# Kernel tuning notes

Measured on AMD Instinct MI355X. Metric: run time of the kernel, lower is better.

## Reference

```python
import jax, jax.numpy as jnp
import numpy as np

N_HEAD = 16

def apply_rope(t, cos, sin):
    # t: [B, H, T, hd]; cos/sin: [T, hd//2] -> broadcast [1,1,T,hd//2]
    hd = t.shape[-1]
    t1, t2 = t[..., : hd // 2], t[..., hd // 2 :]
    c = cos[None, None, :, :]
    s = sin[None, None, :, :]
    return jnp.concatenate([t1 * c - t2 * s, t1 * s + t2 * c], axis=-1)

def setup_inputs() -> dict:
    key = jax.random.key(0)
    k1, k2, k3, k4, k5 = jax.random.split(key, 5)
    B, T, C = 2, 2048, 2048
    hd = C // N_HEAD
    x = jax.random.normal(k1, (B, T, C), dtype=jnp.float32)
    cos = jax.random.uniform(k2, (T, hd // 2), dtype=jnp.float32)
    sin = jax.random.uniform(k3, (T, hd // 2), dtype=jnp.float32)
    W_attn = jax.random.normal(k4, (C, 3 * C), dtype=jnp.float32) * (1.0 / np.sqrt(C))
    W_proj = jax.random.normal(k5, (C, C), dtype=jnp.float32) * (1.0 / np.sqrt(C))
    return {"x": x, "cos": cos, "sin": sin, "W_attn": W_attn, "W_proj": W_proj}

def reference(x, cos, sin, W_attn, W_proj):
    B, T, C = x.shape
    hd = C // N_HEAD
    qkv = jnp.einsum("btc,cd->btd", x, W_attn)  # [B,T,3C]
    q, k, v = jnp.split(qkv, 3, axis=-1)
    # [B,T,C] -> [B,H,T,hd]
    def to_heads(t):
        return t.reshape(B, T, N_HEAD, hd).transpose(0, 2, 1, 3)
    q, k, v = to_heads(q), to_heads(k), to_heads(v)
    q = apply_rope(q, cos[:T], sin[:T])
    k = apply_rope(k, cos[:T], sin[:T])
    scale = 1.0 / np.sqrt(hd).astype(np.float32)
    scores = jnp.einsum("bhqd,bhkd->bhqk", q, k) * scale
    causal = jnp.tril(jnp.ones((T, T), dtype=bool))
    scores = jnp.where(causal[None, None], scores, jnp.finfo(scores.dtype).min)
    attn = jax.nn.softmax(scores, axis=-1)
    y = jnp.einsum("bhqk,bhkd->bhqd", attn, v)  # [B,H,T,hd]
    y = y.transpose(0, 2, 1, 3).reshape(B, T, C)
    return jnp.einsum("btc,cd->btd", y, W_proj)
```

## Files before the change

kernel.cpp:

```cpp
#include <hip/hip_runtime.h>
#include <stdint.h>

typedef unsigned short u16;
typedef __bf16 v8bf __attribute__((ext_vector_type(8)));
typedef float f32x4 __attribute__((ext_vector_type(4)));

#define MFMA16(a, b, c) __builtin_amdgcn_mfma_f32_16x16x32_bf16((a), (b), (c), 0, 0, 0)

typedef const __attribute__((address_space(1))) uint32_t* gp32;
typedef __attribute__((address_space(3))) uint32_t* lp32;
#define ASYNC16(g, l) __builtin_amdgcn_global_load_lds((gp32)(const void*)(g), (lp32)(void*)(l), 16, 0, 0)

__device__ __forceinline__ u16 f2bf(float f) {
  union { float f; uint32_t u; } v; v.f = f;
  uint32_t r = v.u + 0x7fffu + ((v.u >> 16) & 1u);
  return (u16)(r >> 16);
}
__device__ __forceinline__ float bf2f(u16 h) {
  union { uint32_t u; float f; } v; v.u = ((uint32_t)h) << 16;
  return v.f;
}

__device__ __forceinline__ int swK(int r, int lc) {
  return r * 128 + (((lc ^ (r & 7)) & 15) << 3);
}
__device__ __forceinline__ int swV(int r, int lc) {
  return r * 64 + (((lc ^ (r & 7)) & 7) << 3);
}

__global__ __launch_bounds__(256) void cast_x_kernel(const float* __restrict__ in,
                                                     u16* __restrict__ out) {
  int i = (blockIdx.x * 256 + threadIdx.x) * 8;
  float4 a = *(const float4*)(in + i);
  float4 b = *(const float4*)(in + i + 4);
  uint4 o;
  o.x = (uint32_t)f2bf(a.x) | ((uint32_t)f2bf(a.y) << 16);
  o.y = (uint32_t)f2bf(a.z) | ((uint32_t)f2bf(a.w) << 16);
  o.z = (uint32_t)f2bf(b.x) | ((uint32_t)f2bf(b.y) << 16);
  o.w = (uint32_t)f2bf(b.z) | ((uint32_t)f2bf(b.w) << 16);
  *(uint4*)(out + i) = o;
}

__global__ __launch_bounds__(256) void transpose_cast_kernel(const float* __restrict__ in,
                                                             u16* __restrict__ out,
                                                             int R, int Cc) {
  __shared__ u16 tile[32][34];
  int c0 = blockIdx.x * 32, r0 = blockIdx.y * 32;
  int tx = threadIdx.x, ty = threadIdx.y;
#pragma unroll
  for (int i = 0; i < 32; i += 8)
    tile[ty + i][tx] = f2bf(in[(size_t)(r0 + ty + i) * Cc + c0 + tx]);
  __syncthreads();
#pragma unroll
  for (int i = 0; i < 32; i += 8)
    out[(size_t)(c0 + ty + i) * R + r0 + tx] = tile[tx][ty + i];
}

template <typename OutT>
__global__ __launch_bounds__(256) void gemm_bt(const u16* __restrict__ A,
                                               const u16* __restrict__ Bt,
                                               OutT* __restrict__ C, int M, int N, int K) {
  __shared__ u16 As[128 * 64];
  __shared__ u16 Bs[128 * 64];
  int tid = threadIdx.x;
  int wave = tid >> 6, lane = tid & 63, quad = lane >> 4, l16 = lane & 15;
  int wr = wave >> 1, wc = wave & 1;
  int m0 = blockIdx.y * 128, n0 = blockIdx.x * 128;
  f32x4 acc[4][4] = {};
  int lrow = lane >> 3, lk = lane & 7;
  int lc = lk ^ lrow;
  const u16* Ab = A + (size_t)m0 * K;
  const u16* Bb = Bt + (size_t)n0 * K;

  for (int k0 = 0; k0 < K; k0 += 64) {
#pragma unroll
    for (int j = 0; j < 4; ++j) {
      int rbase = wave * 32 + j * 8;
      int row = rbase + lrow;
      ASYNC16(Ab + (size_t)row * K + k0 + lc * 8, &As[rbase * 64]);
      ASYNC16(Bb + (size_t)row * K + k0 + lc * 8, &Bs[rbase * 64]);
    }
    __syncthreads();
#pragma unroll
    for (int ks = 0; ks < 2; ++ks) {
      v8bf af[4], bfr[4];
#pragma unroll
      for (int t = 0; t < 4; ++t) {
        af[t]  = *(const v8bf*)&As[swV(wr * 64 + t * 16 + l16, ks * 4 + quad)];
        bfr[t] = *(const v8bf*)&Bs[swV(wc * 64 + t * 16 + l16, ks * 4 + quad)];
      }
#pragma unroll
      for (int mt = 0; mt < 4; ++mt)
#pragma unroll
        for (int nt = 0; nt < 4; ++nt)
          acc[mt][nt] = MFMA16(af[mt], bfr[nt], acc[mt][nt]);
    }
    __syncthreads();
  }
#pragma unroll
  for (int mt = 0; mt < 4; ++mt)
#pragma unroll
    for (int nt = 0; nt < 4; ++nt) {
      int row = m0 + wr * 64 + mt * 16 + quad * 4;
      int col = n0 + wc * 64 + nt * 16 + l16;
#pragma unroll
      for (int r = 0; r < 4; ++r) {
        float v = acc[mt][nt][r];
        if constexpr (sizeof(OutT) == 2)
          C[(size_t)(row + r) * N + col] = (OutT)f2bf(v);
        else
          C[(size_t)(row + r) * N + col] = v;
      }
    }
}

__global__ __launch_bounds__(256) void rope_repack(const u16* __restrict__ qkv,
                                                   const float* __restrict__ cosp,
                                                   const float* __restrict__ sinp,
                                                   u16* __restrict__ qh, u16* __restrict__ kh,
                                                   u16* __restrict__ vt) {
  __shared__ u16 tile[128 * 130];
  const int T = 2048, C3 = 6144;
  const float QSCL = 0.08838834764831845f * 1.4426950408889634f;
  int t0 = blockIdx.x * 128;
  int bh = blockIdx.y, b = bh >> 4, h = bh & 15;
  int tid = threadIdx.x;
#pragma unroll 2
  for (int i = 0; i < 32; ++i) {
    int e = i * 256 + tid;
    int tl = e >> 6, j = e & 63;
    int t = t0 + tl;
    size_t base = (size_t)(b * T + t) * C3 + h * 128;
    float c = cosp[t * 64 + j], s = sinp[t * 64 + j];
    float q1 = bf2f(qkv[base + j]),        q2 = bf2f(qkv[base + 64 + j]);
    float k1 = bf2f(qkv[base + 2048 + j]), k2 = bf2f(qkv[base + 2048 + 64 + j]);
    size_t o = ((size_t)bh * T + t) * 128;
    qh[o + j]      = f2bf((q1 * c - q2 * s) * QSCL);
    qh[o + 64 + j] = f2bf((q1 * s + q2 * c) * QSCL);
    kh[o + j]      = f2bf(k1 * c - k2 * s);
    kh[o + 64 + j] = f2bf(k1 * s + k2 * c);
  }
#pragma unroll 2
  for (int i = 0; i < 32; ++i) {
    int e = i * 256 + tid;
    int tl = e >> 6, dc = (e & 63) * 2;
    size_t base = (size_t)(b * T + t0 + tl) * C3 + 4096 + h * 128;
    *(uint32_t*)&tile[tl * 130 + dc] = *(const uint32_t*)&qkv[base + dc];
  }
  __syncthreads();
#pragma unroll 2
  for (int i = 0; i < 32; ++i) {
    int e = i * 256 + tid;
    int d = e >> 6, tp = (e & 63) * 2;
    uint32_t v = (uint32_t)tile[tp * 130 + d] | ((uint32_t)tile[(tp + 1) * 130 + d] << 16);
    *(uint32_t*)&vt[((size_t)bh * 128 + d) * T + t0 + tp] = v;
  }
}

__global__ __launch_bounds__(256) void flash_attn(const u16* __restrict__ qh,
                                                  const u16* __restrict__ kh,
                                                  const u16* __restrict__ vt,
                                                  u16* __restrict__ yh) {
  __shared__ u16 Ks[2][64 * 128];
  __shared__ u16 Vs[128 * 64];
  __shared__ u16 Pb[128 * 64];
  const int T = 2048, HD = 128;
  int tid = threadIdx.x;
  int wave = tid >> 6, lane = tid & 63, quad = lane >> 4, l16 = lane & 15;
  int bh = blockIdx.y, b = bh >> 4, h = bh & 15;
  const u16* qb = qh + (size_t)bh * T * HD;
  const u16* kb = kh + (size_t)bh * T * HD;
  const u16* vb = vt + (size_t)bh * HD * T;
  int krow_off = lane >> 4, kchunk = lane & 15;
  int vrow_off = lane >> 3, vchunk = lane & 7;

  for (int tp = 0; tp < 2; ++tp) {
    int qt = tp ? 15 - (int)blockIdx.x : (int)blockIdx.x;
    int q0 = qt * 128;
    int n_it = 2 * qt + 2;

    v8bf qf[2][4];
#pragma unroll
    for (int mt = 0; mt < 2; ++mt)
#pragma unroll
      for (int ks = 0; ks < 4; ++ks)
        qf[mt][ks] = *(const v8bf*)&qb[(size_t)(q0 + wave * 32 + mt * 16 + l16) * HD + ks * 32 + quad * 8];

    f32x4 acc[2][8] = {};
    float rs_p[2][4] = {};
    uint4 vreg[4];

#pragma unroll
    for (int j = 0; j < 4; ++j) {
      int rbase = wave * 16 + j * 4;
      int r = rbase + krow_off;
      int lc = kchunk ^ (r & 7);
      ASYNC16(kb + (size_t)r * HD + lc * 8, &Ks[0][rbase * 128]);
    }
#pragma unroll
    for (int j = 0; j < 4; ++j) {
      int row = wave * 32 + j * 8 + vrow_off;
      int lc = vchunk ^ (row & 7);
      vreg[j] = *(const uint4*)&vb[(size_t)row * T + lc * 8];
    }
    __syncthreads();
#pragma unroll
    for (int j = 0; j < 4; ++j) {
      int row = wave * 32 + j * 8 + vrow_off;
      *(uint4*)&Vs[row * 64 + vchunk * 8] = vreg[j];
    }

    for (int it = 0; it < n_it; ++it) {
      int c = it & 1;
      __syncthreads();

      if (it + 1 < n_it) {
        int kv0n = (it + 1) * 64;
#pragma unroll
        for (int j = 0; j < 4; ++j) {
          int rbase = wave * 16 + j * 4;
          int r = rbase + krow_off;
          int lc = kchunk ^ (r & 7);
          ASYNC16(kb + (size_t)(kv0n + r) * HD + lc * 8, &Ks[1 - c][rbase * 128]);
        }
#pragma unroll
        for (int j = 0; j < 4; ++j) {
          int row = wave * 32 + j * 8 + vrow_off;
          int lc = vchunk ^ (row & 7);
          vreg[j] = *(const uint4*)&vb[(size_t)row * T + kv0n + lc * 8];
        }
      }

      f32x4 s[2][4] = {};
#pragma unroll
      for (int ks = 0; ks < 4; ++ks)
#pragma unroll
        for (int nt = 0; nt < 4; ++nt) {
          v8bf kf = *(const v8bf*)&Ks[c][swK(nt * 16 + l16, ks * 4 + quad)];
          s[0][nt] = MFMA16(qf[0][ks], kf, s[0][nt]);
          s[1][nt] = MFMA16(qf[1][ks], kf, s[1][nt]);
        }

      if (it >= 2 * qt) {
        int kv0 = it * 64;
#pragma unroll
        for (int mt = 0; mt < 2; ++mt)
#pragma unroll
          for (int r = 0; r < 4; ++r) {
            int row = q0 + wave * 32 + mt * 16 + quad * 4 + r;
#pragma unroll
            for (int nt = 0; nt < 4; ++nt)
              if (kv0 + nt * 16 + l16 > row) s[mt][nt][r] = -1e30f;
          }
      }

#pragma unroll
      for (int mt = 0; mt < 2; ++mt)
#pragma unroll
        for (int nt = 0; nt < 4; ++nt)
#pragma unroll
          for (int r = 0; r < 4; ++r) {
            float p = __builtin_exp2f(s[mt][nt][r]);
            rs_p[mt][r] += p;
            int row = wave * 32 + mt * 16 + quad * 4 + r;
            int col = nt * 16 + l16;
            Pb[row * 64 + ((((col >> 3) ^ (row & 7)) & 7) << 3) + (col & 7)] = f2bf(p);
          }

#pragma unroll
      for (int ks = 0; ks < 2; ++ks) {
        v8bf pa0 = *(const v8bf*)&Pb[swV(wave * 32 + l16, ks * 4 + quad)];
        v8bf pa1 = *(const v8bf*)&Pb[swV(wave * 32 + 16 + l16, ks * 4 + quad)];
#pragma unroll
        for (int dt = 0; dt < 8; ++dt) {
          v8bf vf = *(const v8bf*)&Vs[swV(dt * 16 + l16, ks * 4 + quad)];
          acc[0][dt] = MFMA16(pa0, vf, acc[0][dt]);
          acc[1][dt] = MFMA16(pa1, vf, acc[1][dt]);
        }
      }

      __syncthreads();

      if (it + 1 < n_it) {
#pragma unroll
        for (int j = 0; j < 4; ++j) {
          int row = wave * 32 + j * 8 + vrow_off;
          *(uint4*)&Vs[row * 64 + vchunk * 8] = vreg[j];
        }
      }
    }

#pragma unroll
    for (int mt = 0; mt < 2; ++mt)
#pragma unroll
      for (int r = 0; r < 4; ++r) {
        float rsv = rs_p[mt][r];
        rsv += __shfl_xor(rsv, 1);
        rsv += __shfl_xor(rsv, 2);
        rsv += __shfl_xor(rsv, 4);
        rsv += __shfl_xor(rsv, 8);
        float inv = 1.f / rsv;
        int t = q0 + wave * 32 + mt * 16 + quad * 4 + r;
#pragma unroll
        for (int dt = 0; dt < 8; ++dt)
          yh[(size_t)(b * T + t) * 2048 + h * 128 + dt * 16 + l16] = f2bf(acc[mt][dt][r] * inv);
      }
  }
}

extern "C" void kernel_launch(void* const* d_in, const int* in_sizes, int n_in,
                              void* d_out, int out_size, void* d_ws, size_t ws_size,
                              hipStream_t stream) {
  const float* x    = (const float*)d_in[0];
  const float* cosp = (const float*)d_in[1];
  const float* sinp = (const float*)d_in[2];
  const float* Wa   = (const float*)d_in[3];
  const float* Wp   = (const float*)d_in[4];
  float* out = (float*)d_out;

  char* ws = (char*)d_ws;
  u16* xb  = (u16*)(ws);
  u16* WaT = (u16*)(ws + (size_t)(16 << 20));
  u16* WpT = (u16*)(ws + (size_t)(40 << 20));
  u16* qkv = (u16*)(ws + (size_t)(48 << 20));
  u16* qh  = (u16*)(ws + (size_t)(96 << 20));
  u16* kh  = (u16*)(ws + (size_t)(112 << 20));
  u16* vt  = (u16*)(ws + (size_t)(128 << 20));
  u16* yh  = (u16*)(ws + (size_t)(144 << 20));

  cast_x_kernel<<<4096, 256, 0, stream>>>(x, xb);
  transpose_cast_kernel<<<dim3(192, 64), dim3(32, 8), 0, stream>>>(Wa, WaT, 2048, 6144);
  transpose_cast_kernel<<<dim3(64, 64), dim3(32, 8), 0, stream>>>(Wp, WpT, 2048, 2048);
  gemm_bt<u16><<<dim3(48, 32), 256, 0, stream>>>(xb, WaT, qkv, 4096, 6144, 2048);
  rope_repack<<<dim3(16, 32), 256, 0, stream>>>(qkv, cosp, sinp, qh, kh, vt);
  flash_attn<<<dim3(8, 32), 256, 0, stream>>>(qh, kh, vt, yh);
  gemm_bt<float><<<dim3(16, 32), 256, 0, stream>>>(yh, WpT, out, 4096, 2048, 2048);
}
```

Baseline: 427.5 us.

## Split flash attention KV range across two wave groups per block

```diff
diff --git a/kernel.cpp b/kernel.cpp
--- a/kernel.cpp
+++ b/kernel.cpp
@@ -157,77 +157,83 @@
   }
 }
 
-__global__ __launch_bounds__(256) void flash_attn(const u16* __restrict__ qh,
+__global__ __launch_bounds__(512) void flash_attn(const u16* __restrict__ qh,
                                                   const u16* __restrict__ kh,
                                                   const u16* __restrict__ vt,
                                                   u16* __restrict__ yh) {
-  __shared__ u16 Ks[2][64 * 128];
-  __shared__ u16 Vs[128 * 64];
-  __shared__ u16 Pb[128 * 64];
+  __shared__ u16 L[2][32768];
   const int T = 2048, HD = 128;
   int tid = threadIdx.x;
-  int wave = tid >> 6, lane = tid & 63, quad = lane >> 4, l16 = lane & 15;
+  int g = tid >> 8;
+  int gwave = (tid >> 6) & 3;
+  int lane = tid & 63, quad = lane >> 4, l16 = lane & 15;
   int bh = blockIdx.y, b = bh >> 4, h = bh & 15;
   const u16* qb = qh + (size_t)bh * T * HD;
   const u16* kb = kh + (size_t)bh * T * HD;
   const u16* vb = vt + (size_t)bh * HD * T;
+  u16* Ks0 = &L[g][0];
+  u16* Ks1 = &L[g][8192];
+  u16* Vs  = &L[g][16384];
+  u16* Pb  = &L[g][24576];
   int krow_off = lane >> 4, kchunk = lane & 15;
   int vrow_off = lane >> 3, vchunk = lane & 7;
 
   for (int tp = 0; tp < 2; ++tp) {
     int qt = tp ? 15 - (int)blockIdx.x : (int)blockIdx.x;
     int q0 = qt * 128;
-    int n_it = 2 * qt + 2;
+    int n_it = qt + 1;
 
     v8bf qf[2][4];
 #pragma unroll
     for (int mt = 0; mt < 2; ++mt)
 #pragma unroll
       for (int ks = 0; ks < 4; ++ks)
-        qf[mt][ks] = *(const v8bf*)&qb[(size_t)(q0 + wave * 32 + mt * 16 + l16) * HD + ks * 32 + quad * 8];
+        qf[mt][ks] = *(const v8bf*)&qb[(size_t)(q0 + gwave * 32 + mt * 16 + l16) * HD + ks * 32 + quad * 8];
 
     f32x4 acc[2][8] = {};
     float rs_p[2][4] = {};
     uint4 vreg[4];
 
+    int kvb0 = g * 64;
 #pragma unroll
     for (int j = 0; j < 4; ++j) {
-      int rbase = wave * 16 + j * 4;
+      int rbase = gwave * 16 + j * 4;
       int r = rbase + krow_off;
       int lc = kchunk ^ (r & 7);
-      ASYNC16(kb + (size_t)r * HD + lc * 8, &Ks[0][rbase * 128]);
+      ASYNC16(kb + (size_t)(kvb0 + r) * HD + lc * 8, Ks0 + rbase * 128);
     }
 #pragma unroll
     for (int j = 0; j < 4; ++j) {
-      int row = wave * 32 + j * 8 + vrow_off;
+      int row = gwave * 32 + j * 8 + vrow_off;
       int lc = vchunk ^ (row & 7);
-      vreg[j] = *(const uint4*)&vb[(size_t)row * T + lc * 8];
+      vreg[j] = *(const uint4*)&vb[(size_t)row * T + kvb0 + lc * 8];
     }
     __syncthreads();
 #pragma unroll
     for (int j = 0; j < 4; ++j) {
-      int row = wave * 32 + j * 8 + vrow_off;
+      int row = gwave * 32 + j * 8 + vrow_off;
       *(uint4*)&Vs[row * 64 + vchunk * 8] = vreg[j];
     }
 
     for (int it = 0; it < n_it; ++it) {
-      int c = it & 1;
+      u16* Kc = (it & 1) ? Ks1 : Ks0;
+      u16* Kn = (it & 1) ? Ks0 : Ks1;
       __syncthreads();
 
       if (it + 1 < n_it) {
-        int kv0n = (it + 1) * 64;
+        int kvn = (it + 1) * 128 + g * 64;
 #pragma unroll
         for (int j = 0; j < 4; ++j) {
-          int rbase = wave * 16 + j * 4;
+          int rbase = gwave * 16 + j * 4;
           int r = rbase + krow_off;
           int lc = kchunk ^ (r & 7);
-          ASYNC16(kb + (size_t)(kv0n + r) * HD + lc * 8, &Ks[1 - c][rbase * 128]);
+          ASYNC16(kb + (size_t)(kvn + r) * HD + lc * 8, Kn + rbase * 128);
         }
 #pragma unroll
         for (int j = 0; j < 4; ++j) {
-          int row = wave * 32 + j * 8 + vrow_off;
+          int row = gwave * 32 + j * 8 + vrow_off;
           int lc = vchunk ^ (row & 7);
-          vreg[j] = *(const uint4*)&vb[(size_t)row * T + kv0n + lc * 8];
+          vreg[j] = *(const uint4*)&vb[(size_t)row * T + kvn + lc * 8];
         }
       }
 
@@ -236,21 +242,21 @@
       for (int ks = 0; ks < 4; ++ks)
 #pragma unroll
         for (int nt = 0; nt < 4; ++nt) {
-          v8bf kf = *(const v8bf*)&Ks[c][swK(nt * 16 + l16, ks * 4 + quad)];
+          v8bf kf = *(const v8bf*)&Kc[swK(nt * 16 + l16, ks * 4 + quad)];
           s[0][nt] = MFMA16(qf[0][ks], kf, s[0][nt]);
           s[1][nt] = MFMA16(qf[1][ks], kf, s[1][nt]);
         }
 
-      if (it >= 2 * qt) {
-        int kv0 = it * 64;
+      if (it == qt) {
+        int kv0g = it * 128 + g * 64;
 #pragma unroll
         for (int mt = 0; mt < 2; ++mt)
 #pragma unroll
           for (int r = 0; r < 4; ++r) {
-            int row = q0 + wave * 32 + mt * 16 + quad * 4 + r;
+            int row = q0 + gwave * 32 + mt * 16 + quad * 4 + r;
 #pragma unroll
             for (int nt = 0; nt < 4; ++nt)
-              if (kv0 + nt * 16 + l16 > row) s[mt][nt][r] = -1e30f;
+              if (kv0g + nt * 16 + l16 > row) s[mt][nt][r] = -1e30f;
           }
       }
 
@@ -262,15 +268,15 @@
           for (int r = 0; r < 4; ++r) {
             float p = __builtin_exp2f(s[mt][nt][r]);
             rs_p[mt][r] += p;
-            int row = wave * 32 + mt * 16 + quad * 4 + r;
+            int row = gwave * 32 + mt * 16 + quad * 4 + r;
             int col = nt * 16 + l16;
             Pb[row * 64 + ((((col >> 3) ^ (row & 7)) & 7) << 3) + (col & 7)] = f2bf(p);
           }
 
 #pragma unroll
       for (int ks = 0; ks < 2; ++ks) {
-        v8bf pa0 = *(const v8bf*)&Pb[swV(wave * 32 + l16, ks * 4 + quad)];
-        v8bf pa1 = *(const v8bf*)&Pb[swV(wave * 32 + 16 + l16, ks * 4 + quad)];
+        v8bf pa0 = *(const v8bf*)&Pb[swV(gwave * 32 + l16, ks * 4 + quad)];
+        v8bf pa1 = *(const v8bf*)&Pb[swV(gwave * 32 + 16 + l16, ks * 4 + quad)];
 #pragma unroll
         for (int dt = 0; dt < 8; ++dt) {
           v8bf vf = *(const v8bf*)&Vs[swV(dt * 16 + l16, ks * 4 + quad)];
@@ -284,27 +290,55 @@
       if (it + 1 < n_it) {
 #pragma unroll
         for (int j = 0; j < 4; ++j) {
-          int row = wave * 32 + j * 8 + vrow_off;
+          int row = gwave * 32 + j * 8 + vrow_off;
           *(uint4*)&Vs[row * 64 + vchunk * 8] = vreg[j];
         }
       }
     }
 
+    float rsv[2][4];
 #pragma unroll
     for (int mt = 0; mt < 2; ++mt)
 #pragma unroll
       for (int r = 0; r < 4; ++r) {
-        float rsv = rs_p[mt][r];
-        rsv += __shfl_xor(rsv, 1);
-        rsv += __shfl_xor(rsv, 2);
-        rsv += __shfl_xor(rsv, 4);
-        rsv += __shfl_xor(rsv, 8);
-        float inv = 1.f / rsv;
-        int t = q0 + wave * 32 + mt * 16 + quad * 4 + r;
-#pragma unroll
-        for (int dt = 0; dt < 8; ++dt)
-          yh[(size_t)(b * T + t) * 2048 + h * 128 + dt * 16 + l16] = f2bf(acc[mt][dt][r] * inv);
-      }
+        float v = rs_p[mt][r];
+        v += __shfl_xor(v, 1);
+        v += __shfl_xor(v, 2);
+        v += __shfl_xor(v, 4);
+        v += __shfl_xor(v, 8);
+        rsv[mt][r] = v;
+      }
+    float* Lacc = (float*)&L[1][0];
+    float* Lrs  = (float*)&L[0][24576];
+    if (g == 1) {
+#pragma unroll
+      for (int mt = 0; mt < 2; ++mt)
+#pragma unroll
+        for (int r = 0; r < 4; ++r) {
+          int row = gwave * 32 + mt * 16 + quad * 4 + r;
+#pragma unroll
+          for (int dt = 0; dt < 8; ++dt)
+            Lacc[row * 128 + dt * 16 + l16] = acc[mt][dt][r];
+          if (l16 == 0) Lrs[row] = rsv[mt][r];
+        }
+    }
+    __syncthreads();
+    if (g == 0) {
+#pragma unroll
+      for (int mt = 0; mt < 2; ++mt)
+#pragma unroll
+        for (int r = 0; r < 4; ++r) {
+          int row = gwave * 32 + mt * 16 + quad * 4 + r;
+          float inv = 1.f / (rsv[mt][r] + Lrs[row]);
+          int t = q0 + row;
+#pragma unroll
+          for (int dt = 0; dt < 8; ++dt) {
+            float o = acc[mt][dt][r] + Lacc[row * 128 + dt * 16 + l16];
+            yh[(size_t)(b * T + t) * 2048 + h * 128 + dt * 16 + l16] = f2bf(o * inv);
+          }
+        }
+    }
+    __syncthreads();
   }
 }
 
@@ -333,6 +367,6 @@
   transpose_cast_kernel<<<dim3(64, 64), dim3(32, 8), 0, stream>>>(Wp, WpT, 2048, 2048);
   gemm_bt<u16><<<dim3(48, 32), 256, 0, stream>>>(xb, WaT, qkv, 4096, 6144, 2048);
   rope_repack<<<dim3(16, 32), 256, 0, stream>>>(qkv, cosp, sinp, qh, kh, vt);
-  flash_attn<<<dim3(8, 32), 256, 0, stream>>>(qh, kh, vt, yh);
+  flash_attn<<<dim3(8, 32), 512, 0, stream>>>(qh, kh, vt, yh);
   gemm_bt<float><<<dim3(16, 32), 256, 0, stream>>>(yh, WpT, out, 4096, 2048, 2048);
 }
```

Measured after the change: 431.3 us. About the same (+0.9%).
